# Kernel tuning notes

Hardware: AMD Instinct MI355X
Metric: run time of the kernel (lower is better)

## Reference

```python
import jax, jax.numpy as jnp
import numpy as np

EPS = 1e-6
HEADS = 4


def _gather(x, idx):
    # x: (b,n,...), idx: (b,n,k) -> (b,n,k,...)
    return jax.vmap(lambda xb, ib: xb[ib])(x, idx)


def _prenorm(f0, f1):
    # FiberNorm: layernorm on scalars, norm-based RMS normalization on vectors
    mu = jnp.mean(f0, -1, keepdims=True)
    var = jnp.var(f0, -1, keepdims=True)
    g0 = (f0 - mu) * jax.lax.rsqrt(var + EPS)
    n1 = jnp.sum(f1 * f1, -1)  # (b,n,d1) squared channel norms
    rms = jax.lax.rsqrt(jnp.mean(n1, -1, keepdims=True) + EPS)  # (b,n,1)
    g1 = f1 * rms[..., None]
    return g0, g1


def _forward(f0, f1, coords, nbr_idx, Wq0, Wq1, Wk00, Wk10, Wk01, Wk11, Wk11r,
             Wv00, Wv10, Wv01, Wv11, Wv11r, Rw1, Rb1, Rw20, Rw21, Wo0, Wo1,
             F0w1, F0w2, F1w1, F1w2):
    b, n, d0 = f0.shape
    d1 = f1.shape[2]
    k = nbr_idx.shape[-1]
    L = Wq0.shape[0]
    # equivariant basis ingredients: relative positions over neighbor graph
    rel = _gather(coords, nbr_idx) - coords[:, :, None, :]       # (b,n,k,3)
    dist = jnp.linalg.norm(rel, axis=-1, keepdims=True)          # (b,n,k,1)
    rhat = rel / (dist + EPS)                                    # (b,n,k,3)
    scale = 1.0 / np.sqrt(d0 // HEADS + 3 * (d1 // HEADS)).astype(np.float32)
    for l in range(L):
        # ---- attention block (prenorm -> TFN attention -> residual) ----
        g0, g1 = _prenorm(f0, f1)
        rh = jax.nn.gelu(dist @ Rw1[l] + Rb1[l])                 # radial MLP (b,n,k,rh)
        r0 = rh @ Rw20[l]                                        # (b,n,k,d0)
        r1 = rh @ Rw21[l]                                        # (b,n,k,d1)
        q0 = g0 @ Wq0[l]                                         # (b,n,d0)
        q1 = jnp.einsum('bncm,ce->bnem', g1, Wq1[l])             # (b,n,d1,3)
        h0 = _gather(g0, nbr_idx)                                # (b,n,k,d0)
        h1 = _gather(g1, nbr_idx)                                # (b,n,k,d1,3)
        dot1 = jnp.einsum('bnkcm,bnkm->bnkc', h1, rhat)          # deg1->deg0 basis contraction
        k0 = (h0 @ Wk00[l] + dot1 @ Wk10[l]) * r0
        v0 = (h0 @ Wv00[l] + dot1 @ Wv10[l]) * r0
        rh_e = rhat[:, :, :, None, :]                            # (b,n,k,1,3)
        k1 = (jnp.einsum('bnkc,ce->bnke', h0, Wk01[l])[..., None] * rh_e
              + jnp.einsum('bnkcm,ce->bnkem', h1, Wk11[l])
              + jnp.einsum('bnkc,ce->bnke', dot1, Wk11r[l])[..., None] * rh_e) * r1[..., None]
        v1 = (jnp.einsum('bnkc,ce->bnke', h0, Wv01[l])[..., None] * rh_e
              + jnp.einsum('bnkcm,ce->bnkem', h1, Wv11[l])
              + jnp.einsum('bnkc,ce->bnke', dot1, Wv11r[l])[..., None] * rh_e) * r1[..., None]
        # multi-head invariant attention logits over neighbors
        hq0 = q0.reshape(b, n, HEADS, -1)
        hk0 = k0.reshape(b, n, k, HEADS, -1)
        hq1 = q1.reshape(b, n, HEADS, -1, 3)
        hk1 = k1.reshape(b, n, k, HEADS, -1, 3)
        logits = (jnp.einsum('bnhc,bnkhc->bnkh', hq0, hk0)
                  + jnp.einsum('bnhcm,bnkhcm->bnkh', hq1, hk1)) * scale
        a = jax.nn.softmax(logits, axis=2)                       # over neighbors
        o0 = jnp.einsum('bnkh,bnkhc->bnhc', a, v0.reshape(b, n, k, HEADS, -1)).reshape(b, n, d0)
        o1 = jnp.einsum('bnkh,bnkhcm->bnhcm', a, v1.reshape(b, n, k, HEADS, -1, 3)).reshape(b, n, d1, 3)
        f0 = f0 + o0 @ Wo0[l]
        f1 = f1 + jnp.einsum('bncm,ce->bnem', o1, Wo1[l])
        # ---- feedforward residual block (prenorm -> fiber FF -> residual) ----
        g0, g1 = _prenorm(f0, f1)
        f0 = f0 + jax.nn.gelu(g0 @ F0w1[l]) @ F0w2[l]
        u1 = jnp.einsum('bncm,ce->bnem', g1, F1w1[l])            # (b,n,4*d1,3)
        gate = jax.nn.sigmoid(jnp.linalg.norm(u1, axis=-1))     # norm-gated equivariant nonlin
        u1 = u1 * gate[..., None]
        f1 = f1 + jnp.einsum('bnem,ef->bnfm', u1, F1w2[l])
    return jnp.concatenate([f0, f1.reshape(b, n, d1 * 3)], axis=-1)


def setup_inputs() -> dict:
    key = jax.random.key(0)
    ks = iter(jax.random.split(key, 40))
    b, n, k, d0, d1, L, rh = 2, 4096, 32, 64, 16, 2, 16
    def w(shape, fan):
        return jax.random.normal(next(ks), shape, jnp.float32) / np.sqrt(fan).astype(np.float32)
    inp = {
        'f0': jax.random.normal(next(ks), (b, n, d0), jnp.float32),
        'f1': jax.random.normal(next(ks), (b, n, d1, 3), jnp.float32),
        'coords': jax.random.normal(next(ks), (b, n, 3), jnp.float32),
        'nbr_idx': jax.random.randint(next(ks), (b, n, k), 0, n),
        'Wq0': w((L, d0, d0), d0), 'Wq1': w((L, d1, d1), d1),
        'Wk00': w((L, d0, d0), d0), 'Wk10': w((L, d1, d0), d1),
        'Wk01': w((L, d0, d1), d0), 'Wk11': w((L, d1, d1), d1), 'Wk11r': w((L, d1, d1), d1),
        'Wv00': w((L, d0, d0), d0), 'Wv10': w((L, d1, d0), d1),
        'Wv01': w((L, d0, d1), d0), 'Wv11': w((L, d1, d1), d1), 'Wv11r': w((L, d1, d1), d1),
        'Rw1': w((L, 1, rh), 1), 'Rb1': jnp.zeros((L, rh), jnp.float32),
        'Rw20': w((L, rh, d0), rh), 'Rw21': w((L, rh, d1), rh),
        'Wo0': w((L, d0, d0), d0), 'Wo1': w((L, d1, d1), d1),
        'F0w1': w((L, d0, 4 * d0), d0), 'F0w2': w((L, 4 * d0, d0), 4 * d0),
        'F1w1': w((L, d1, 4 * d1), d1), 'F1w2': w((L, 4 * d1, d1), 4 * d1),
    }
    return inp


def reference(f0, f1, coords, nbr_idx, Wq0, Wq1, Wk00, Wk10, Wk01, Wk11, Wk11r,
              Wv00, Wv10, Wv01, Wv11, Wv11r, Rw1, Rb1, Rw20, Rw21, Wo0, Wo1,
              F0w1, F0w2, F1w1, F1w2):
    return _forward(f0, f1, coords, nbr_idx, Wq0, Wq1, Wk00, Wk10, Wk01, Wk11,
                    Wk11r, Wv00, Wv10, Wv01, Wv11, Wv11r, Rw1, Rb1, Rw20, Rw21,
                    Wo0, Wo1, F0w1, F0w2, F1w1, F1w2)
```

## Files before the change

### kernel.cpp

```cpp
#include <hip/hip_runtime.h>
#include <math.h>

#define BB    2
#define NN    4096
#define KK    32
#define D0    64
#define D1    16
#define D13   48
#define RHD   16
#define NHEAD 4
#define NLAYER 2
#define EPS   1e-6f
#define SCALE 0.18898223650461363f
#define ETOT  (BB*NN*KK)

typedef float  f32x4 __attribute__((ext_vector_type(4)));
typedef short  s16x8 __attribute__((ext_vector_type(8)));
#define MFMA16(a,b,c) __builtin_amdgcn_mfma_f32_16x16x32_bf16(a,b,c,0,0,0)

__device__ __forceinline__ unsigned short f2bf(float x) {
    union { float f; unsigned u; } v; v.f = x;
    unsigned r = v.u + 0x7fffu + ((v.u >> 16) & 1u);
    return (unsigned short)(r >> 16);
}
__device__ __forceinline__ float bf2f(unsigned short h) {
    union { unsigned u; float f; } v; v.u = ((unsigned)h) << 16;
    return v.f;
}
__device__ __forceinline__ void split_bf(float x, unsigned short* hi, unsigned short* lo) {
    unsigned short h = f2bf(x);
    *hi = h;
    *lo = f2bf(x - bf2f(h));
}

__device__ __forceinline__ f32x4 mm3(s16x8 ah, s16x8 al, s16x8 bh, s16x8 bl, f32x4 c) {
    c = MFMA16(ah, bh, c);
    c = MFMA16(ah, bl, c);
    c = MFMA16(al, bh, c);
    return c;
}

__device__ __forceinline__ float wred(float v) {
    #pragma unroll
    for (int o = 32; o > 0; o >>= 1) v += __shfl_xor(v, o, 64);
    return v;
}

__device__ __forceinline__ float gelu_t(float x) {
    float x3 = x * x * x;
    return 0.5f * x * (1.0f + tanhf(0.7978845608028654f * (x + 0.044715f * x3)));
}

__global__ void geom_kernel(const float* __restrict__ coords,
                            const int* __restrict__ nbr,
                            float* __restrict__ rhat,
                            float* __restrict__ dist) {
    int e = blockIdx.x * blockDim.x + threadIdx.x;
    if (e >= ETOT) return;
    int bn = e / KK;
    int bb = bn / NN;
    int j  = nbr[e];
    const float* cs = coords + (size_t)bn * 3;
    const float* cn = coords + ((size_t)bb * NN + j) * 3;
    float rx = cn[0] - cs[0], ry = cn[1] - cs[1], rz = cn[2] - cs[2];
    float d  = sqrtf(rx * rx + ry * ry + rz * rz);
    float iv = 1.0f / (d + EPS);
    rhat[e * 3 + 0] = rx * iv;
    rhat[e * 3 + 1] = ry * iv;
    rhat[e * 3 + 2] = rz * iv;
    dist[e] = d;
}

__global__ __launch_bounds__(64) void prenorm_q_kernel(
    const float* __restrict__ f0, const float* __restrict__ f1,
    const float* __restrict__ Wq0, const float* __restrict__ Wq1,
    float* __restrict__ g1,
    float* __restrict__ q0, float* __restrict__ q1,
    unsigned short* __restrict__ g0H, unsigned short* __restrict__ g0L,
    unsigned short* __restrict__ g1mH, unsigned short* __restrict__ g1mL) {
    int node = blockIdx.x;
    int lane = threadIdx.x;
    __shared__ float g0s[D0], g1s[D13];

    float x  = f0[(size_t)node * D0 + lane];
    float mu = wred(x) * (1.0f / D0);
    float dv = x - mu;
    float var = wred(dv * dv) * (1.0f / D0);
    float g0v = dv * rsqrtf(var + EPS);
    split_bf(g0v, &g0H[(size_t)node * D0 + lane], &g0L[(size_t)node * D0 + lane]);
    g0s[lane] = g0v;

    float w = (lane < D13) ? f1[(size_t)node * D13 + lane] : 0.0f;
    float t = wred(w * w);
    float rms = rsqrtf(t * (1.0f / D1) + EPS);
    if (lane < D13) {
        float g1v = w * rms;
        g1[(size_t)node * D13 + lane] = g1v;
        g1s[lane] = g1v;
        int c = lane / 3, m = lane % 3;
        split_bf(g1v, &g1mH[(size_t)node * D13 + m * 16 + c],
                      &g1mL[(size_t)node * D13 + m * 16 + c]);
    }
    __syncthreads();

    float acc = 0.0f;
    #pragma unroll
    for (int c = 0; c < D0; c++) acc += g0s[c] * Wq0[c * D0 + lane];
    q0[(size_t)node * D0 + lane] = acc;
    if (lane < D13) {
        int e = lane / 3, m = lane % 3;
        float a1 = 0.0f;
        #pragma unroll
        for (int c = 0; c < D1; c++) a1 += g1s[c * 3 + m] * Wq1[c * D1 + e];
        q1[(size_t)node * D13 + lane] = a1;
    }
}

__global__ __launch_bounds__(256) void edge_prep_kernel(
    const int* __restrict__ nbr,
    const float* __restrict__ rhatb, const float* __restrict__ distb,
    const float* __restrict__ g1b,
    const float* __restrict__ Rw1, const float* __restrict__ Rb1,
    unsigned short* __restrict__ d1H, unsigned short* __restrict__ d1L,
    unsigned short* __restrict__ rhHg, unsigned short* __restrict__ rhLg) {
    int t = blockIdx.x * 256 + threadIdx.x;
    int e = t >> 4, c = t & 15;
    int bn = e >> 5;
    int bb = bn >> 12;
    int nj = nbr[e];
    const float* g1 = g1b + ((size_t)bb * NN + nj) * D13 + c * 3;
    float d1 = g1[0] * rhatb[e * 3] + g1[1] * rhatb[e * 3 + 1] + g1[2] * rhatb[e * 3 + 2];
    split_bf(d1, &d1H[t], &d1L[t]);
    float rh = gelu_t(distb[e] * Rw1[c] + Rb1[c]);
    split_bf(rh, &rhHg[t], &rhLg[t]);
}

__device__ __forceinline__ float B1val(int n, int k,
    const float* Wk00, const float* Wk10, const float* Wv00, const float* Wv10) {
    int nn = n & 63;
    const float* W0 = (n < 64) ? Wk00 : Wv00;
    const float* W1 = (n < 64) ? Wk10 : Wv10;
    if (k < 64) return W0[k * D0 + nn];
    if (k < 80) return W1[(k - 64) * D0 + nn];
    return 0.0f;
}
__device__ __forceinline__ float B2val(int n, int k,
    const float* Wk01, const float* Wk11, const float* Wk11r,
    const float* Wv01, const float* Wv11, const float* Wv11r) {
    if (n < 16) {
        if (k < 64) return Wk01[k * D1 + n];
        if (k < 80) return Wk11r[(k - 64) * D1 + n];
        return 0.0f;
    }
    if (n < 32) {
        int e = n - 16;
        if (k < 64) return Wv01[k * D1 + e];
        if (k < 80) return Wv11r[(k - 64) * D1 + e];
        return 0.0f;
    }
    if (n < 80) {
        int m = (n - 32) >> 4, e = (n - 32) & 15;
        if (k >= 80) { int mm = (k - 80) >> 4, c = (k - 80) & 15; if (mm == m) return Wk11[c * D1 + e]; }
        return 0.0f;
    }
    { int m = (n - 80) >> 4, e = (n - 80) & 15;
      if (k >= 80) { int mm = (k - 80) >> 4, c = (k - 80) & 15; if (mm == m) return Wv11[c * D1 + e]; }
      return 0.0f; }
}

__global__ void prep_kernel(
    const float* __restrict__ Wk00, const float* __restrict__ Wk10,
    const float* __restrict__ Wk01, const float* __restrict__ Wk11,
    const float* __restrict__ Wk11r,
    const float* __restrict__ Wv00, const float* __restrict__ Wv10,
    const float* __restrict__ Wv01, const float* __restrict__ Wv11,
    const float* __restrict__ Wv11r,
    const float* __restrict__ Rw20, const float* __restrict__ Rw21,
    unsigned short* __restrict__ B1H, unsigned short* __restrict__ B1L,
    unsigned short* __restrict__ B2H, unsigned short* __restrict__ B2L,
    unsigned short* __restrict__ R0H, unsigned short* __restrict__ R0L,
    unsigned short* __restrict__ R1H, unsigned short* __restrict__ R1L) {
    int gid = blockIdx.x * 256 + threadIdx.x;
    if (gid >= 2 * 3904) return;
    int l  = (gid >= 3904) ? 1 : 0;
    int id = gid - l * 3904;
    const float* Wk00l = Wk00 + l * D0 * D0;
    const float* Wk10l = Wk10 + l * D1 * D0;
    const float* Wk01l = Wk01 + l * D0 * D1;
    const float* Wk11l = Wk11 + l * D1 * D1;
    const float* Wk11rl= Wk11r+ l * D1 * D1;
    const float* Wv00l = Wv00 + l * D0 * D0;
    const float* Wv10l = Wv10 + l * D1 * D0;
    const float* Wv01l = Wv01 + l * D0 * D1;
    const float* Wv11l = Wv11 + l * D1 * D1;
    const float* Wv11rl= Wv11r+ l * D1 * D1;
    const float* Rw20l = Rw20 + l * RHD * D0;
    const float* Rw21l = Rw21 + l * RHD * D1;
    unsigned short* B1Hl = B1H + l * 1536 * 8;
    unsigned short* B1Ll = B1L + l * 1536 * 8;
    unsigned short* B2Hl = B2H + l * 2048 * 8;
    unsigned short* B2Ll = B2L + l * 2048 * 8;
    unsigned short* R0Hl = R0H + l * 256 * 8;
    unsigned short* R0Ll = R0L + l * 256 * 8;
    unsigned short* R1Hl = R1H + l * 64 * 8;
    unsigned short* R1Ll = R1L + l * 64 * 8;

    if (id < 1536) {
        int ks = id >> 9, rem = id & 511, nt = rem >> 6, lane = rem & 63;
        int li = lane & 15, quad = lane >> 4;
        #pragma unroll
        for (int t = 0; t < 8; t++) {
            float v = B1val(nt * 16 + li, ks * 32 + quad * 8 + t, Wk00l, Wk10l, Wv00l, Wv10l);
            split_bf(v, &B1Hl[id * 8 + t], &B1Ll[id * 8 + t]);
        }
    } else if (id < 3584) {
        int id2 = id - 1536;
        int ks = id2 >> 9, rem = id2 & 511, nt = rem >> 6, lane = rem & 63;
        int li = lane & 15, quad = lane >> 4;
        #pragma unroll
        for (int t = 0; t < 8; t++) {
            float v = B2val(nt * 16 + li, ks * 32 + quad * 8 + t,
                            Wk01l, Wk11l, Wk11rl, Wv01l, Wv11l, Wv11rl);
            split_bf(v, &B2Hl[id2 * 8 + t], &B2Ll[id2 * 8 + t]);
        }
    } else if (id < 3840) {
        int id2 = id - 3584;
        int nt = id2 >> 6, lane = id2 & 63;
        int li = lane & 15, quad = lane >> 4;
        #pragma unroll
        for (int t = 0; t < 8; t++) {
            int k = quad * 8 + t;
            float v = (k < 16) ? Rw20l[k * D0 + nt * 16 + li] : 0.0f;
            split_bf(v, &R0Hl[id2 * 8 + t], &R0Ll[id2 * 8 + t]);
        }
    } else {
        int id2 = id - 3840;
        int li = id2 & 15, quad = id2 >> 4;
        #pragma unroll
        for (int t = 0; t < 8; t++) {
            int k = quad * 8 + t;
            float v = (k < 16) ? Rw21l[k * D1 + li] : 0.0f;
            split_bf(v, &R1Hl[id2 * 8 + t], &R1Ll[id2 * 8 + t]);
        }
    }
}

__global__ __launch_bounds__(64) void attn_fused_kernel(
    const int* __restrict__ nbr_idx,
    const float* __restrict__ rhatg,
    const float* __restrict__ q0g, const float* __restrict__ q1g,
    const unsigned short* __restrict__ g0H, const unsigned short* __restrict__ g0L,
    const unsigned short* __restrict__ g1mH, const unsigned short* __restrict__ g1mL,
    const unsigned short* __restrict__ d1H, const unsigned short* __restrict__ d1L,
    const unsigned short* __restrict__ rhHg, const unsigned short* __restrict__ rhLg,
    const unsigned short* __restrict__ B1H, const unsigned short* __restrict__ B1L,
    const unsigned short* __restrict__ B2H, const unsigned short* __restrict__ B2L,
    const unsigned short* __restrict__ R0H, const unsigned short* __restrict__ R0L,
    const unsigned short* __restrict__ R1H, const unsigned short* __restrict__ R1L,
    const float* __restrict__ Wo0, const float* __restrict__ Wo1,
    float* __restrict__ f0b, float* __restrict__ f1b) {

    int B0    = blockIdx.x * 64;
    int node0 = blockIdx.x * 2;
    int bb    = node0 >> 12;
    int lane  = threadIdx.x;
    int li    = lane & 15, quad = lane >> 4;
    int koff  = quad * 8;

    __shared__ float rhts[192];
    __shared__ float lgs0[64][4];
    __shared__ float lgs1[64][4];
    __shared__ float v0s[64][68];
    __shared__ float v1s[64][49];
    __shared__ float o0s[2][D0];
    __shared__ float o1s[2][D13];

    rhts[lane]       = rhatg[(size_t)B0 * 3 + lane];
    rhts[lane + 64]  = rhatg[(size_t)B0 * 3 + lane + 64];
    rhts[lane + 128] = rhatg[(size_t)B0 * 3 + lane + 128];
    __syncthreads();

    size_t em[4], nm[4];
    #pragma unroll
    for (int mt = 0; mt < 4; mt++) {
        em[mt] = (size_t)B0 + mt * 16 + li;
        nm[mt] = (size_t)bb * NN + nbr_idx[em[mt]];
    }

    #define APTRS(ks, nb, ee, PH, PL)                                              \
        const unsigned short *PH, *PL;                                             \
        if (ks < 2) {                                                              \
            PH = g0H + (nb) * 64 + ks * 32 + koff;                                 \
            PL = g0L + (nb) * 64 + ks * 32 + koff;                                 \
        } else if (ks == 2) {                                                      \
            PH = (quad < 2) ? d1H + (ee) * 16 + quad * 8                           \
                            : g1mH + (nb) * 48 + (quad - 2) * 8;                   \
            PL = (quad < 2) ? d1L + (ee) * 16 + quad * 8                           \
                            : g1mL + (nb) * 48 + (quad - 2) * 8;                   \
        } else {                                                                   \
            PH = (quad < 2) ? g1mH + (nb) * 48 + 16 + quad * 8                     \
                            : g1mH + (nb) * 48 + 32 + (quad - 2) * 8;              \
            PL = (quad < 2) ? g1mL + (nb) * 48 + 16 + quad * 8                     \
                            : g1mL + (nb) * 48 + 32 + (quad - 2) * 8;              \
        }

    f32x4 acc[4][8];

    #pragma unroll
    for (int i = 0; i < 4; i++)
        #pragma unroll
        for (int j = 0; j < 8; j++) acc[i][j] = (f32x4){0.f, 0.f, 0.f, 0.f};
    #pragma unroll
    for (int ks = 0; ks < 3; ks++) {
        s16x8 ah[4], al[4];
        #pragma unroll
        for (int mt = 0; mt < 4; mt++) {
            APTRS(ks, nm[mt], em[mt], pH, pL)
            ah[mt] = *(const s16x8*)pH;
            al[mt] = *(const s16x8*)pL;
        }
        #pragma unroll
        for (int nt = 0; nt < 8; nt++) {
            s16x8 bh = *(const s16x8*)(B1H + ((ks * 8 + nt) * 64 + lane) * 8);
            s16x8 bl = *(const s16x8*)(B1L + ((ks * 8 + nt) * 64 + lane) * 8);
            #pragma unroll
            for (int mt = 0; mt < 4; mt++)
                acc[mt][nt] = mm3(ah[mt], al[mt], bh, bl, acc[mt][nt]);
        }
    }

    {
        f32x4 r0a[4][4];
        #pragma unroll
        for (int i = 0; i < 4; i++)
            #pragma unroll
            for (int j = 0; j < 4; j++) r0a[i][j] = (f32x4){0.f, 0.f, 0.f, 0.f};
        s16x8 zz = (s16x8){0,0,0,0,0,0,0,0};
        s16x8 rah[4], ral[4];
        #pragma unroll
        for (int mt = 0; mt < 4; mt++) {
            rah[mt] = zz; ral[mt] = zz;
            if (quad < 2) {
                rah[mt] = *(const s16x8*)(rhHg + em[mt] * 16 + koff);
                ral[mt] = *(const s16x8*)(rhLg + em[mt] * 16 + koff);
            }
        }
        #pragma unroll
        for (int nt = 0; nt < 4; nt++) {
            s16x8 bh = *(const s16x8*)(R0H + (nt * 64 + lane) * 8);
            s16x8 bl = *(const s16x8*)(R0L + (nt * 64 + lane) * 8);
            #pragma unroll
            for (int mt = 0; mt < 4; mt++)
                r0a[mt][nt] = mm3(rah[mt], ral[mt], bh, bl, r0a[mt][nt]);
        }

        float q0e[2][4];
        #pragma unroll
        for (int nw = 0; nw < 2; nw++)
            #pragma unroll
            for (int nt = 0; nt < 4; nt++)
                q0e[nw][nt] = q0g[(size_t)(node0 + nw) * D0 + nt * 16 + li];
        #pragma unroll
        for (int mt = 0; mt < 4; mt++) {
            int nw = mt >> 1;
            float p0[4][4];
            #pragma unroll
            for (int nt = 0; nt < 4; nt++)
                #pragma unroll
                for (int r = 0; r < 4; r++)
                    p0[nt][r] = q0e[nw][nt] * (acc[mt][nt][r] * r0a[mt][nt][r]);
            #pragma unroll
            for (int off = 1; off < 16; off <<= 1) {
                #pragma unroll
                for (int nt = 0; nt < 4; nt++)
                    #pragma unroll
                    for (int r = 0; r < 4; r++)
                        p0[nt][r] += __shfl_xor(p0[nt][r], off, 16);
            }
            if (li == 0) {
                int jb = mt * 16 + quad * 4;
                #pragma unroll
                for (int r = 0; r < 4; r++)
                    #pragma unroll
                    for (int nt = 0; nt < 4; nt++)
                        lgs0[jb + r][nt] = p0[nt][r];
            }
            #pragma unroll
            for (int nt = 0; nt < 4; nt++)
                #pragma unroll
                for (int r = 0; r < 4; r++)
                    v0s[mt * 16 + quad * 4 + r][nt * 16 + li] =
                        acc[mt][nt + 4][r] * r0a[mt][nt][r];
        }
    }

    f32x4 r1a[4];
    {
        s16x8 zz = (s16x8){0,0,0,0,0,0,0,0};
        s16x8 bh = *(const s16x8*)(R1H + lane * 8);
        s16x8 bl = *(const s16x8*)(R1L + lane * 8);
        #pragma unroll
        for (int mt = 0; mt < 4; mt++) {
            s16x8 rah = zz, ral = zz;
            if (quad < 2) {
                rah = *(const s16x8*)(rhHg + em[mt] * 16 + koff);
                ral = *(const s16x8*)(rhLg + em[mt] * 16 + koff);
            }
            r1a[mt] = (f32x4){0.f, 0.f, 0.f, 0.f};
            r1a[mt] = mm3(rah, ral, bh, bl, r1a[mt]);
        }
    }

    #pragma unroll
    for (int i = 0; i < 4; i++)
        #pragma unroll
        for (int j = 0; j < 8; j++) acc[i][j] = (f32x4){0.f, 0.f, 0.f, 0.f};
    #pragma unroll
    for (int ks = 0; ks < 4; ks++) {
        s16x8 ah[4], al[4];
        #pragma unroll
        for (int mt = 0; mt < 4; mt++) {
            APTRS(ks, nm[mt], em[mt], pH, pL)
            ah[mt] = *(const s16x8*)pH;
            al[mt] = *(const s16x8*)pL;
        }
        #pragma unroll
        for (int nt = 0; nt < 8; nt++) {
            s16x8 bh = *(const s16x8*)(B2H + ((ks * 8 + nt) * 64 + lane) * 8);
            s16x8 bl = *(const s16x8*)(B2L + ((ks * 8 + nt) * 64 + lane) * 8);
            #pragma unroll
            for (int mt = 0; mt < 4; mt++)
                acc[mt][nt] = mm3(ah[mt], al[mt], bh, bl, acc[mt][nt]);
        }
    }

    {
        float q1v[2][3];
        #pragma unroll
        for (int nw = 0; nw < 2; nw++)
            #pragma unroll
            for (int m = 0; m < 3; m++)
                q1v[nw][m] = q1g[(size_t)(node0 + nw) * D13 + li * 3 + m];
        #pragma unroll
        for (int mt = 0; mt < 4; mt++) {
            int nw = mt >> 1;
            #pragma unroll
            for (int r = 0; r < 4; r++) {
                int j = mt * 16 + quad * 4 + r;
                float r1  = r1a[mt][r];
                float rh0 = rhts[j * 3], rh1 = rhts[j * 3 + 1], rh2 = rhts[j * 3 + 2];
                float sk = acc[mt][0][r], sv = acc[mt][1][r];
                float k1a = (sk * rh0 + acc[mt][2][r]) * r1;
                float k1b = (sk * rh1 + acc[mt][3][r]) * r1;
                float k1c = (sk * rh2 + acc[mt][4][r]) * r1;
                v1s[j][li * 3 + 0] = (sv * rh0 + acc[mt][5][r]) * r1;
                v1s[j][li * 3 + 1] = (sv * rh1 + acc[mt][6][r]) * r1;
                v1s[j][li * 3 + 2] = (sv * rh2 + acc[mt][7][r]) * r1;
                float lc = q1v[nw][0] * k1a + q1v[nw][1] * k1b + q1v[nw][2] * k1c;
                lc += __shfl_xor(lc, 1, 4);
                lc += __shfl_xor(lc, 2, 4);
                if ((li & 3) == 0) lgs1[j][li >> 2] = lc;
            }
        }
    }
    __syncthreads();

    {
        float4 a4 = *(const float4*)&lgs0[lane][0];
        float4 b4 = *(const float4*)&lgs1[lane][0];
        float4 l4;
        l4.x = (a4.x + b4.x) * SCALE; l4.y = (a4.y + b4.y) * SCALE;
        l4.z = (a4.z + b4.z) * SCALE; l4.w = (a4.w + b4.w) * SCALE;
        float4 mx = l4;
        #pragma unroll
        for (int off = 1; off < 32; off <<= 1) {
            mx.x = fmaxf(mx.x, __shfl_xor(mx.x, off, 32));
            mx.y = fmaxf(mx.y, __shfl_xor(mx.y, off, 32));
            mx.z = fmaxf(mx.z, __shfl_xor(mx.z, off, 32));
            mx.w = fmaxf(mx.w, __shfl_xor(mx.w, off, 32));
        }
        float4 ex;
        ex.x = expf(l4.x - mx.x); ex.y = expf(l4.y - mx.y);
        ex.z = expf(l4.z - mx.z); ex.w = expf(l4.w - mx.w);
        float4 s = ex;
        #pragma unroll
        for (int off = 1; off < 32; off <<= 1) {
            s.x += __shfl_xor(s.x, off, 32);
            s.y += __shfl_xor(s.y, off, 32);
            s.z += __shfl_xor(s.z, off, 32);
            s.w += __shfl_xor(s.w, off, 32);
        }
        ex.x /= s.x; ex.y /= s.y; ex.z /= s.z; ex.w /= s.w;
        *(float4*)&lgs0[lane][0] = ex;
    }
    __syncthreads();

    {
        int h0 = lane >> 4;
        #pragma unroll
        for (int nw = 0; nw < 2; nw++) {
            float p = 0.0f;
            #pragma unroll
            for (int jn = 0; jn < KK; jn++)
                p += lgs0[nw * 32 + jn][h0] * v0s[nw * 32 + jn][lane];
            o0s[nw][lane] = p;
        }
    }
    if (lane < D13) {
        int h1 = (lane / 3) >> 2;
        #pragma unroll
        for (int nw = 0; nw < 2; nw++) {
            float p = 0.0f;
            #pragma unroll
            for (int jn = 0; jn < KK; jn++)
                p += lgs0[nw * 32 + jn][h1] * v1s[nw * 32 + jn][lane];
            o1s[nw][lane] = p;
        }
    }
    __syncthreads();

    #pragma unroll
    for (int nw = 0; nw < 2; nw++) {
        float a0 = 0.0f;
        #pragma unroll
        for (int e = 0; e < D0; e++) a0 += o0s[nw][e] * Wo0[e * D0 + lane];
        f0b[(size_t)(node0 + nw) * D0 + lane] += a0;
    }
    if (lane < D13) {
        int f = lane / 3, m = lane % 3;
        #pragma unroll
        for (int nw = 0; nw < 2; nw++) {
            float a1 = 0.0f;
            #pragma unroll
            for (int c = 0; c < D1; c++) a1 += o1s[nw][c * 3 + m] * Wo1[c * D1 + f];
            f1b[(size_t)(node0 + nw) * D13 + lane] += a1;
        }
    }
    #undef APTRS
}

__global__ __launch_bounds__(256) void ffn_kernel(
    const float* __restrict__ F0w1, const float* __restrict__ F0w2,
    const float* __restrict__ F1w1, const float* __restrict__ F1w2,
    float* __restrict__ f0b, float* __restrict__ f1b,
    int last,
    const float* __restrict__ Wq0n, const float* __restrict__ Wq1n,
    float* __restrict__ g1b, float* __restrict__ q0b, float* __restrict__ q1b,
    unsigned short* __restrict__ g0H, unsigned short* __restrict__ g0L,
    unsigned short* __restrict__ g1mH, unsigned short* __restrict__ g1mL,
    float* __restrict__ out) {
    int w    = threadIdx.x >> 6, lane = threadIdx.x & 63;
    int node = blockIdx.x * 4 + w;

    __shared__ float g0s[4][D0];
    __shared__ float g1s[4][D13];
    __shared__ float ts[4][256];
    __shared__ float us[4][192];

    float f0old = f0b[(size_t)node * D0 + lane];
    float f1old = (lane < D13) ? f1b[(size_t)node * D13 + lane] : 0.0f;

    {
        float mu = wred(f0old) * (1.0f / D0);
        float dv = f0old - mu;
        float var = wred(dv * dv) * (1.0f / D0);
        g0s[w][lane] = dv * rsqrtf(var + EPS);

        float t = wred(f1old * f1old);
        float rms = rsqrtf(t * (1.0f / D1) + EPS);
        if (lane < D13) g1s[w][lane] = f1old * rms;
    }
    __syncthreads();

    #pragma unroll
    for (int u = 0; u < 4; u++) {
        int h = u * 64 + lane;
        float acc = 0.0f;
        #pragma unroll
        for (int c = 0; c < D0; c++) acc += g0s[w][c] * F0w1[c * 256 + h];
        ts[w][h] = gelu_t(acc);
    }
    #pragma unroll
    for (int u = 0; u < 3; u++) {
        int t = u * 64 + lane;
        int e = t / 3, m = t % 3;
        float acc = 0.0f;
        #pragma unroll
        for (int c = 0; c < D1; c++) acc += g1s[w][c * 3 + m] * F1w1[c * 64 + e];
        us[w][t] = acc;
    }
    __syncthreads();

    {
        float a = us[w][lane * 3], b = us[w][lane * 3 + 1], c = us[w][lane * 3 + 2];
        float nrm = sqrtf(a * a + b * b + c * c);
        float gate = 1.0f / (1.0f + expf(-nrm));
        us[w][lane * 3 + 0] = a * gate;
        us[w][lane * 3 + 1] = b * gate;
        us[w][lane * 3 + 2] = c * gate;
    }
    __syncthreads();

    float f0new;
    {
        float acc = 0.0f;
        #pragma unroll 8
        for (int j = 0; j < 256; j++) acc += ts[w][j] * F0w2[j * D0 + lane];
        f0new = f0old + acc;
    }
    float f1new = f1old;
    if (lane < D13) {
        int f = lane / 3, m = lane % 3;
        float acc = 0.0f;
        #pragma unroll
        for (int e = 0; e < 64; e++) acc += us[w][e * 3 + m] * F1w2[e * D1 + f];
        f1new = f1old + acc;
    }

    if (last) {
        out[(size_t)node * (D0 + D13) + lane] = f0new;
        if (lane < D13) out[(size_t)node * (D0 + D13) + D0 + lane] = f1new;
        return;
    }

    f0b[(size_t)node * D0 + lane] = f0new;
    if (lane < D13) f1b[(size_t)node * D13 + lane] = f1new;

    float mu = wred(f0new) * (1.0f / D0);
    float dv = f0new - mu;
    float var = wred(dv * dv) * (1.0f / D0);
    float g0v = dv * rsqrtf(var + EPS);
    split_bf(g0v, &g0H[(size_t)node * D0 + lane], &g0L[(size_t)node * D0 + lane]);
    float w1v = (lane < D13) ? f1new : 0.0f;
    float t2 = wred(w1v * w1v);
    float rms2 = rsqrtf(t2 * (1.0f / D1) + EPS);
    g0s[w][lane] = g0v;
    if (lane < D13) {
        float g1v = w1v * rms2;
        g1b[(size_t)node * D13 + lane] = g1v;
        g1s[w][lane] = g1v;
        int c = lane / 3, m = lane % 3;
        split_bf(g1v, &g1mH[(size_t)node * D13 + m * 16 + c],
                      &g1mL[(size_t)node * D13 + m * 16 + c]);
    }
    __syncthreads();

    {
        float acc = 0.0f;
        #pragma unroll
        for (int c = 0; c < D0; c++) acc += g0s[w][c] * Wq0n[c * D0 + lane];
        q0b[(size_t)node * D0 + lane] = acc;
    }
    if (lane < D13) {
        int e = lane / 3, m = lane % 3;
        float a1 = 0.0f;
        #pragma unroll
        for (int c = 0; c < D1; c++) a1 += g1s[w][c * 3 + m] * Wq1n[c * D1 + e];
        q1b[(size_t)node * D13 + lane] = a1;
    }
}

extern "C" void kernel_launch(void* const* d_in, const int* in_sizes, int n_in,
                              void* d_out, int out_size, void* d_ws, size_t ws_size,
                              hipStream_t stream) {
    const float* f0     = (const float*)d_in[0];
    const float* f1     = (const float*)d_in[1];
    const float* coords = (const float*)d_in[2];
    const int*   nbr    = (const int*)d_in[3];
    const float* Wq0    = (const float*)d_in[4];
    const float* Wq1    = (const float*)d_in[5];
    const float* Wk00   = (const float*)d_in[6];
    const float* Wk10   = (const float*)d_in[7];
    const float* Wk01   = (const float*)d_in[8];
    const float* Wk11   = (const float*)d_in[9];
    const float* Wk11r  = (const float*)d_in[10];
    const float* Wv00   = (const float*)d_in[11];
    const float* Wv10   = (const float*)d_in[12];
    const float* Wv01   = (const float*)d_in[13];
    const float* Wv11   = (const float*)d_in[14];
    const float* Wv11r  = (const float*)d_in[15];
    const float* Rw1    = (const float*)d_in[16];
    const float* Rb1    = (const float*)d_in[17];
    const float* Rw20   = (const float*)d_in[18];
    const float* Rw21   = (const float*)d_in[19];
    const float* Wo0    = (const float*)d_in[20];
    const float* Wo1    = (const float*)d_in[21];
    const float* F0w1   = (const float*)d_in[22];
    const float* F0w2   = (const float*)d_in[23];
    const float* F1w1   = (const float*)d_in[24];
    const float* F1w2   = (const float*)d_in[25];
    float* out = (float*)d_out;

    int nodes = BB * NN;

    float* wf = (float*)d_ws;
    float* f0b   = wf; wf += (size_t)nodes * D0;
    float* f1b   = wf; wf += (size_t)nodes * D13;
    float* g1b   = wf; wf += (size_t)nodes * D13;
    float* q0b   = wf; wf += (size_t)nodes * D0;
    float* q1b   = wf; wf += (size_t)nodes * D13;
    float* rhatb = wf; wf += (size_t)ETOT * 3;
    float* distb = wf; wf += (size_t)ETOT;
    unsigned short* wu = (unsigned short*)wf;
    unsigned short* g0H  = wu; wu += (size_t)nodes * D0;
    unsigned short* g0L  = wu; wu += (size_t)nodes * D0;
    unsigned short* g1mH = wu; wu += (size_t)nodes * D13;
    unsigned short* g1mL = wu; wu += (size_t)nodes * D13;
    unsigned short* d1H  = wu; wu += (size_t)ETOT * 16;
    unsigned short* d1L  = wu; wu += (size_t)ETOT * 16;
    unsigned short* rhH  = wu; wu += (size_t)ETOT * 16;
    unsigned short* rhL  = wu; wu += (size_t)ETOT * 16;
    unsigned short* B1H = wu; wu += 2 * 1536 * 8;
    unsigned short* B1L = wu; wu += 2 * 1536 * 8;
    unsigned short* B2H = wu; wu += 2 * 2048 * 8;
    unsigned short* B2L = wu; wu += 2 * 2048 * 8;
    unsigned short* R0H = wu; wu += 2 * 256 * 8;
    unsigned short* R0L = wu; wu += 2 * 256 * 8;
    unsigned short* R1H = wu; wu += 2 * 64 * 8;
    unsigned short* R1L = wu; wu += 2 * 64 * 8;

    geom_kernel<<<(ETOT + 255) / 256, 256, 0, stream>>>(coords, nbr, rhatb, distb);
    hipMemcpyAsync(f0b, f0, (size_t)nodes * D0 * sizeof(float),
                   hipMemcpyDeviceToDevice, stream);
    hipMemcpyAsync(f1b, f1, (size_t)nodes * D13 * sizeof(float),
                   hipMemcpyDeviceToDevice, stream);

    prep_kernel<<<(2 * 3904 + 255) / 256, 256, 0, stream>>>(
        Wk00, Wk10, Wk01, Wk11, Wk11r, Wv00, Wv10, Wv01, Wv11, Wv11r,
        Rw20, Rw21, B1H, B1L, B2H, B2L, R0H, R0L, R1H, R1L);

    prenorm_q_kernel<<<nodes, 64, 0, stream>>>(
        f0b, f1b, Wq0, Wq1, g1b, q0b, q1b, g0H, g0L, g1mH, g1mL);

    for (int l = 0; l < NLAYER; l++) {
        int last = (l == NLAYER - 1);
        int ln   = last ? 0 : (l + 1);
        edge_prep_kernel<<<ETOT * 16 / 256, 256, 0, stream>>>(
            nbr, rhatb, distb, g1b, Rw1 + l * RHD, Rb1 + l * RHD,
            d1H, d1L, rhH, rhL);
        attn_fused_kernel<<<ETOT / 64, 64, 0, stream>>>(
            nbr, rhatb, q0b, q1b,
            g0H, g0L, g1mH, g1mL, d1H, d1L, rhH, rhL,
            B1H + l * 1536 * 8, B1L + l * 1536 * 8,
            B2H + l * 2048 * 8, B2L + l * 2048 * 8,
            R0H + l * 256 * 8,  R0L + l * 256 * 8,
            R1H + l * 64 * 8,   R1L + l * 64 * 8,
            Wo0 + l * D0 * D0, Wo1 + l * D1 * D1,
            f0b, f1b);
        ffn_kernel<<<nodes / 4, 256, 0, stream>>>(
            F0w1 + l * D0 * 256, F0w2 + l * 256 * D0,
            F1w1 + l * D1 * 64, F1w2 + l * 64 * D1,
            f0b, f1b, last,
            Wq0 + ln * D0 * D0, Wq1 + ln * D1 * D1,
            g1b, q0b, q1b, g0H, g0L, g1mH, g1mL, out);
    }
}
```

Baseline: 450.8 us.

## Pack two waves per attention block and store V tiles in bf16 shared memory

The fused attention kernel now runs two independent 64-lane waves per 128-thread block, each handling its own pair of nodes, with every shared array given a per-wave index. The v0/v1 staging buffers in shared memory change from fp32 to bf16, roughly halving LDS use per wave so more waves fit per CU. The aim is higher occupancy and less LDS traffic in the attention-weighted sum. The cost is rounding V to bf16, which reduces accuracy compared with the earlier split hi/lo bf16 precision scheme, and the block-wide __syncthreads calls now make the two waves wait on each other.

Result: slower. 501.9 us (+11.3%).

```diff
diff --git a/kernel.cpp b/kernel.cpp
--- a/kernel.cpp
+++ b/kernel.cpp
@@ -245,7 +245,7 @@
     }
 }
 
-__global__ __launch_bounds__(64) void attn_fused_kernel(
+__global__ __launch_bounds__(128) void attn_fused_kernel(
     const int* __restrict__ nbr_idx,
     const float* __restrict__ rhatg,
     const float* __restrict__ q0g, const float* __restrict__ q1g,
@@ -260,24 +260,25 @@
     const float* __restrict__ Wo0, const float* __restrict__ Wo1,
     float* __restrict__ f0b, float* __restrict__ f1b) {
 
-    int B0    = blockIdx.x * 64;
-    int node0 = blockIdx.x * 2;
+    int w     = threadIdx.x >> 6;
+    int lane  = threadIdx.x & 63;
+    int B0    = blockIdx.x * 128 + w * 64;
+    int node0 = blockIdx.x * 4 + w * 2;
     int bb    = node0 >> 12;
-    int lane  = threadIdx.x;
     int li    = lane & 15, quad = lane >> 4;
     int koff  = quad * 8;
 
-    __shared__ float rhts[192];
-    __shared__ float lgs0[64][4];
-    __shared__ float lgs1[64][4];
-    __shared__ float v0s[64][68];
-    __shared__ float v1s[64][49];
-    __shared__ float o0s[2][D0];
-    __shared__ float o1s[2][D13];
-
-    rhts[lane]       = rhatg[(size_t)B0 * 3 + lane];
-    rhts[lane + 64]  = rhatg[(size_t)B0 * 3 + lane + 64];
-    rhts[lane + 128] = rhatg[(size_t)B0 * 3 + lane + 128];
+    __shared__ float rhts[2][192];
+    __shared__ float lgs0[2][64][4];
+    __shared__ float lgs1[2][64][4];
+    __shared__ unsigned short v0h[2][64][72];
+    __shared__ unsigned short v1h[2][64][52];
+    __shared__ float o0s[2][2][D0];
+    __shared__ float o1s[2][2][D13];
+
+    rhts[w][lane]       = rhatg[(size_t)B0 * 3 + lane];
+    rhts[w][lane + 64]  = rhatg[(size_t)B0 * 3 + lane + 64];
+    rhts[w][lane + 128] = rhatg[(size_t)B0 * 3 + lane + 128];
     __syncthreads();
 
     size_t em[4], nm[4];
@@ -383,14 +384,14 @@
                 for (int r = 0; r < 4; r++)
                     #pragma unroll
                     for (int nt = 0; nt < 4; nt++)
-                        lgs0[jb + r][nt] = p0[nt][r];
+                        lgs0[w][jb + r][nt] = p0[nt][r];
             }
             #pragma unroll
             for (int nt = 0; nt < 4; nt++)
                 #pragma unroll
                 for (int r = 0; r < 4; r++)
-                    v0s[mt * 16 + quad * 4 + r][nt * 16 + li] =
-                        acc[mt][nt + 4][r] * r0a[mt][nt][r];
+                    v0h[w][mt * 16 + quad * 4 + r][nt * 16 + li] =
+                        f2bf(acc[mt][nt + 4][r] * r0a[mt][nt][r]);
         }
     }
 
@@ -448,26 +449,26 @@
             for (int r = 0; r < 4; r++) {
                 int j = mt * 16 + quad * 4 + r;
                 float r1  = r1a[mt][r];
-                float rh0 = rhts[j * 3], rh1 = rhts[j * 3 + 1], rh2 = rhts[j * 3 + 2];
+                float rh0 = rhts[w][j * 3], rh1 = rhts[w][j * 3 + 1], rh2 = rhts[w][j * 3 + 2];
                 float sk = acc[mt][0][r], sv = acc[mt][1][r];
                 float k1a = (sk * rh0 + acc[mt][2][r]) * r1;
                 float k1b = (sk * rh1 + acc[mt][3][r]) * r1;
                 float k1c = (sk * rh2 + acc[mt][4][r]) * r1;
-                v1s[j][li * 3 + 0] = (sv * rh0 + acc[mt][5][r]) * r1;
-                v1s[j][li * 3 + 1] = (sv * rh1 + acc[mt][6][r]) * r1;
-                v1s[j][li * 3 + 2] = (sv * rh2 + acc[mt][7][r]) * r1;
+                v1h[w][j][li * 3 + 0] = f2bf((sv * rh0 + acc[mt][5][r]) * r1);
+                v1h[w][j][li * 3 + 1] = f2bf((sv * rh1 + acc[mt][6][r]) * r1);
+                v1h[w][j][li * 3 + 2] = f2bf((sv * rh2 + acc[mt][7][r]) * r1);
                 float lc = q1v[nw][0] * k1a + q1v[nw][1] * k1b + q1v[nw][2] * k1c;
                 lc += __shfl_xor(lc, 1, 4);
                 lc += __shfl_xor(lc, 2, 4);
-                if ((li & 3) == 0) lgs1[j][li >> 2] = lc;
+                if ((li & 3) == 0) lgs1[w][j][li >> 2] = lc;
             }
         }
     }
     __syncthreads();
 
     {
-        float4 a4 = *(const float4*)&lgs0[lane][0];
-        float4 b4 = *(const float4*)&lgs1[lane][0];
+        float4 a4 = *(const float4*)&lgs0[w][lane][0];
+        float4 b4 = *(const float4*)&lgs1[w][lane][0];
         float4 l4;
         l4.x = (a4.x + b4.x) * SCALE; l4.y = (a4.y + b4.y) * SCALE;
         l4.z = (a4.z + b4.z) * SCALE; l4.w = (a4.w + b4.w) * SCALE;
@@ -491,7 +492,7 @@
             s.w += __shfl_xor(s.w, off, 32);
         }
         ex.x /= s.x; ex.y /= s.y; ex.z /= s.z; ex.w /= s.w;
-        *(float4*)&lgs0[lane][0] = ex;
+        *(float4*)&lgs0[w][lane][0] = ex;
     }
     __syncthreads();
 
@@ -502,8 +503,8 @@
             float p = 0.0f;
             #pragma unroll
             for (int jn = 0; jn < KK; jn++)
-                p += lgs0[nw * 32 + jn][h0] * v0s[nw * 32 + jn][lane];
-            o0s[nw][lane] = p;
+                p += lgs0[w][nw * 32 + jn][h0] * bf2f(v0h[w][nw * 32 + jn][lane]);
+            o0s[w][nw][lane] = p;
         }
     }
     if (lane < D13) {
@@ -513,8 +514,8 @@
             float p = 0.0f;
             #pragma unroll
             for (int jn = 0; jn < KK; jn++)
-                p += lgs0[nw * 32 + jn][h1] * v1s[nw * 32 + jn][lane];
-            o1s[nw][lane] = p;
+                p += lgs0[w][nw * 32 + jn][h1] * bf2f(v1h[w][nw * 32 + jn][lane]);
+            o1s[w][nw][lane] = p;
         }
     }
     __syncthreads();
@@ -523,7 +524,7 @@
     for (int nw = 0; nw < 2; nw++) {
         float a0 = 0.0f;
         #pragma unroll
-        for (int e = 0; e < D0; e++) a0 += o0s[nw][e] * Wo0[e * D0 + lane];
+        for (int e = 0; e < D0; e++) a0 += o0s[w][nw][e] * Wo0[e * D0 + lane];
         f0b[(size_t)(node0 + nw) * D0 + lane] += a0;
     }
     if (lane < D13) {
@@ -532,7 +533,7 @@
         for (int nw = 0; nw < 2; nw++) {
             float a1 = 0.0f;
             #pragma unroll
-            for (int c = 0; c < D1; c++) a1 += o1s[nw][c * 3 + m] * Wo1[c * D1 + f];
+            for (int c = 0; c < D1; c++) a1 += o1s[w][nw][c * 3 + m] * Wo1[c * D1 + f];
             f1b[(size_t)(node0 + nw) * D13 + lane] += a1;
         }
     }
@@ -738,7 +739,7 @@
         edge_prep_kernel<<<ETOT * 16 / 256, 256, 0, stream>>>(
             nbr, rhatb, distb, g1b, Rw1 + l * RHD, Rb1 + l * RHD,
             d1H, d1L, rhH, rhL);
-        attn_fused_kernel<<<ETOT / 64, 64, 0, stream>>>(
+        attn_fused_kernel<<<ETOT / 128, 128, 0, stream>>>(
             nbr, rhatb, q0b, q1b,
             g0H, g0L, g1mH, g1mL, d1H, d1L, rhH, rhL,
             B1H + l * 1536 * 8, B1L + l * 1536 * 8,
```
